# Optimization experiments

Measured on AMD Instinct MI355X. Metric: run time of the kernel, lower is better.

The kernel has to match this reference:

```python
import jax, jax.numpy as jnp
import numpy as np
from jax import lax

WSIZE = 11
SIGMA = 1.5
PAD = WSIZE // 2  # 5
C1 = 0.01 ** 2
C2 = 0.03 ** 2


def _gauss1d():
    x = np.arange(WSIZE) - WSIZE // 2
    g = np.exp(-(x.astype(np.float64) ** 2) / (2.0 * SIGMA ** 2))
    g = g / g.sum()
    return jnp.asarray(g, dtype=jnp.float32)


def _blur3d(x, g):
    """Replicate-pad by 5 on D/H/W then apply the separable 11x11x11 Gaussian.
    x: [N, 1, D, H, W]. Mathematically identical to the dense conv3d in the
    original (the 3D window is an exact outer product of the 1D Gaussian)."""
    xp = jnp.pad(x, ((0, 0), (0, 0), (PAD, PAD), (PAD, PAD), (PAD, PAD)), mode='edge')
    dn = ('NCDHW', 'OIDHW', 'NCDHW')
    for kshape in ((1, 1, WSIZE, 1, 1), (1, 1, 1, WSIZE, 1), (1, 1, 1, 1, WSIZE)):
        xp = lax.conv_general_dilated(xp, g.reshape(kshape), (1, 1, 1), 'VALID',
                                      dimension_numbers=dn)
    return xp


def _rerange(img):
    img = jnp.where(img.max() > 128.0, img / 255.0, img)
    img = jnp.where(img.min() < -0.5, (img + 1.0) / 2.0, img)
    return img


def setup_inputs() -> dict:
    key = jax.random.key(0)
    k1, k2 = jax.random.split(key)
    N, C, H, W = 4, 16, 512, 512
    pred = jax.random.uniform(k1, (N, C, H, W), dtype=jnp.float32)
    gt = jax.random.uniform(k2, (N, C, H, W), dtype=jnp.float32)
    return {"pred": pred, "gt": gt}


def reference(pred, gt):
    N = pred.shape[0]
    pred = _rerange(pred)
    gt = _rerange(gt)

    # ---- PSNR (range = 1.0, reduce='sum') ----
    mse = jnp.mean((pred - gt) ** 2, axis=(1, 2, 3))           # [N]
    psnr = jnp.sum(10.0 * jnp.log10(1.0 / mse))                # scalar

    # ---- 3D SSIM over [N,1,C,H,W] volumes ----
    g = _gauss1d()
    img = pred[:, None]                                        # [N,1,D,H,W]
    gtt = gt[:, None]
    mu1 = _blur3d(img, g)
    mu2 = _blur3d(gtt, g)
    mu1_sq = mu1 * mu1
    mu2_sq = mu2 * mu2
    mu1_mu2 = mu1 * mu2
    sigma1_sq = _blur3d(img * img, g) - mu1_sq
    sigma2_sq = _blur3d(gtt * gtt, g) - mu2_sq
    sigma12 = _blur3d(img * gtt, g) - mu1_mu2

    v1 = 2.0 * sigma12 + C2
    v2 = sigma1_sq + sigma2_sq + C2
    ssim_map = ((2.0 * mu1_mu2 + C1) * v1) / ((mu1_sq + mu2_sq + C1) * v2)
    ssim = jnp.sum(jnp.mean(ssim_map, axis=(1, 2, 3, 4)))      # reduce='sum'

    return psnr, ssim, N
```

## Files before the change

### kernel.cpp

```cpp
#include <hip/hip_runtime.h>
#include <cmath>


#define NB 4
#define DD 16
#define HH 512
#define WW 512
#define SLICE (HH * WW)
#define VOL (DD * SLICE)
#define C1F 0.0001f
#define C2F 0.0009f

#define TH 16
#define TW 16
#define SCOLS 26
#define NRP 13
#define PW 14
#define PLSTR 28
#define SDW (NRP * PLSTR)
#define TMW (TH * PW)
#define NTHR 256
#define SIT (NRP * SCOLS)
#define XTRA (SIT - NTHR)
#define HITEMS 104

typedef _Float16 h2v __attribute__((ext_vector_type(2)));

struct KArg {
  unsigned ge[6], go[6];
  unsigned wl2[DD * DD];
};

__device__ inline float dot2h(unsigned a, unsigned b, float c) {
#if __has_builtin(__builtin_amdgcn_fdot2)
  return __builtin_amdgcn_fdot2(__builtin_bit_cast(h2v, a),
                                __builtin_bit_cast(h2v, b), c, false);
#else
  h2v av = __builtin_bit_cast(h2v, a), bv = __builtin_bit_cast(h2v, b);
  return fmaf((float)av.y, (float)bv.y, fmaf((float)av.x, (float)bv.x, c));
#endif
}
__device__ inline unsigned pkh(float a, float b) {
  return __builtin_bit_cast(unsigned, __builtin_amdgcn_cvt_pkrtz(a, b));
}
__device__ inline unsigned pk2sq(unsigned a) {
  h2v v = __builtin_bit_cast(h2v, a);
  v = v * v;
  return __builtin_bit_cast(unsigned, v);
}
__device__ inline int iclamp(int v, int lo, int hi) {
  return v < lo ? lo : (v > hi ? hi : v);
}

__device__ inline float block_sum256(float v) {
#pragma unroll
  for (int o = 32; o > 0; o >>= 1) v += __shfl_down(v, o, 64);
  __shared__ float r[4];
  if ((threadIdx.x & 63) == 0) r[threadIdx.x >> 6] = v;
  __syncthreads();
  float out = 0.f;
  if (threadIdx.x == 0) {
#pragma unroll
    for (int i = 0; i < 4; ++i) out += r[i];
  }
  __syncthreads();
  return out;
}

__global__ void zero_acc_k(float* acc) {
  if (threadIdx.x < 8) acc[threadIdx.x] = 0.f;
}

__global__ __launch_bounds__(NTHR, 3) void fused_k(
    const float* __restrict__ pred, const float* __restrict__ gt,
    float* __restrict__ acc, KArg ka) {
  __shared__ uint2 sd[SDW];
  __shared__ uint4 tmp[TMW];

  int b0 = blockIdx.x;
  int b = (b0 & 7) * ((NB * 1024) >> 3) + (b0 >> 3);
  int tile = b & 1023;
  int n = b >> 10;
  int th0 = (tile >> 5) * TH;
  int tw0 = (tile & 31) * TW;
  int t = threadIdx.x;

  int rp0 = t / SCOLS, x0 = t - rp0 * SCOLS;
  int gx0 = iclamp(tw0 + x0 - 5, 0, WW - 1);
  int go0a = iclamp(th0 + 2 * rp0 - 5, 0, HH - 1) * WW + gx0;
  int go0b = iclamp(th0 + 2 * rp0 - 4, 0, HH - 1) * WW + gx0;
  int w0i = (2 * rp0 + (x0 & 1)) * PW + (x0 >> 1);
  bool ox0 = (x0 >= 5) && (x0 < 5 + TW);
  float o0a = (ox0 && rp0 >= 3 && rp0 <= 10) ? 1.f : 0.f;
  float o0b = (ox0 && rp0 >= 2 && rp0 <= 9) ? 1.f : 0.f;
  int i1 = t + XTRA;
  bool has2 = (i1 >= NTHR);
  int rp1 = i1 / SCOLS, x1 = i1 - rp1 * SCOLS;
  int gx1 = iclamp(tw0 + x1 - 5, 0, WW - 1);
  int go1a = iclamp(th0 + 2 * rp1 - 5, 0, HH - 1) * WW + gx1;
  int go1b = iclamp(th0 + 2 * rp1 - 4, 0, HH - 1) * WW + gx1;
  int w1i = (2 * rp1 + (x1 & 1)) * PW + (x1 >> 1);
  bool ox1 = (x1 >= 5) && (x1 < 5 + TW);
  float o1a = (ox1 && rp1 >= 3 && rp1 <= 10) ? 1.f : 0.f;
  float o1b = (ox1 && rp1 >= 2 && rp1 <= 9) ? 1.f : 0.f;

  bool hasH = (t < HITEMS);
  int hm = t & 7, hcp = t >> 3;
  int hrd = hm * PLSTR + hcp;
  int hwr = (2 * hm) * PW + hcp;

  int wx = t & 15;
  int wrd = (t >> 4) * PW + (wx >> 1);
  unsigned cw[6];
#pragma unroll
  for (int J = 0; J < 6; ++J) cw[J] = (wx & 1) ? ka.go[J] : ka.ge[J];

  const float* pb = pred + (size_t)n * VOL;
  const float* qb = gt + (size_t)n * VOL;

  float p0a = pb[go0a], p0b = pb[go0b], q0a = qb[go0a], q0b = qb[go0b];
  float p1a = 0.f, p1b = 0.f, q1a = 0.f, q1b = 0.f;
  if (has2) { p1a = pb[go1a]; p1b = pb[go1b]; q1a = qb[go1a]; q1b = qb[go1b]; }

  float psnr = 0.f;
  h2v A01[DD], A23[DD];
#pragma unroll
  for (int j = 0; j < DD; ++j) {
    A01[j] = (h2v){(_Float16)0, (_Float16)0};
    A23[j] = (h2v){(_Float16)0, (_Float16)0};
  }

#pragma unroll 1
  for (int d = 0; d < DD; ++d) {
    {
      float SA = p0a + q0a, DA = p0a - q0a;
      float SB = p0b + q0b, DB = p0b - q0b;
      psnr = fmaf(o0a, DA * DA, psnr);
      psnr = fmaf(o0b, DB * DB, psnr);
      sd[w0i] = make_uint2(pkh(SA, SB), pkh(DA, DB));
    }
    if (has2) {
      float SA = p1a + q1a, DA = p1a - q1a;
      float SB = p1b + q1b, DB = p1b - q1b;
      psnr = fmaf(o1a, DA * DA, psnr);
      psnr = fmaf(o1b, DB * DB, psnr);
      sd[w1i] = make_uint2(pkh(SA, SB), pkh(DA, DB));
    }
    __syncthreads();

    if (d < DD - 1) {
      const float* P = pb + (size_t)(d + 1) * SLICE;
      const float* Q = qb + (size_t)(d + 1) * SLICE;
      p0a = P[go0a]; p0b = P[go0b]; q0a = Q[go0a]; q0b = Q[go0b];
      if (has2) { p1a = P[go1a]; p1b = P[go1b]; q1a = Q[go1a]; q1b = Q[go1b]; }
    }

    if (hasH) {
      float e0[4] = {0, 0, 0, 0}, e1[4] = {0, 0, 0, 0};
      float r0[4] = {0, 0, 0, 0}, r1[4] = {0, 0, 0, 0};
#pragma unroll
      for (int J = 0; J < 6; ++J) {
        uint2 ve = sd[hrd + J * PLSTR];
        uint2 vo = sd[hrd + J * PLSTR + PW];
        unsigned ves = pk2sq(ve.x), ved = pk2sq(ve.y);
        unsigned vos = pk2sq(vo.x), vod = pk2sq(vo.y);
        unsigned cge = ka.ge[J], cgo = ka.go[J];
        e0[0] = dot2h(cge, ve.x, e0[0]); e0[1] = dot2h(cge, ve.y, e0[1]);
        e0[2] = dot2h(cge, ves, e0[2]);  e0[3] = dot2h(cge, ved, e0[3]);
        r0[0] = dot2h(cgo, ve.x, r0[0]); r0[1] = dot2h(cgo, ve.y, r0[1]);
        r0[2] = dot2h(cgo, ves, r0[2]);  r0[3] = dot2h(cgo, ved, r0[3]);
        e1[0] = dot2h(cge, vo.x, e1[0]); e1[1] = dot2h(cge, vo.y, e1[1]);
        e1[2] = dot2h(cge, vos, e1[2]);  e1[3] = dot2h(cge, vod, e1[3]);
        r1[0] = dot2h(cgo, vo.x, r1[0]); r1[1] = dot2h(cgo, vo.y, r1[1]);
        r1[2] = dot2h(cgo, vos, r1[2]);  r1[3] = dot2h(cgo, vod, r1[3]);
      }
      tmp[hwr] = make_uint4(pkh(e0[0], e1[0]), pkh(e0[1], e1[1]),
                            pkh(e0[2], e1[2]), pkh(e0[3], e1[3]));
      tmp[hwr + PW] = make_uint4(pkh(r0[0], r1[0]), pkh(r0[1], r1[1]),
                                 pkh(r0[2], r1[2]), pkh(r0[3], r1[3]));
    }
    __syncthreads();

    float w0 = 0.f, w1 = 0.f, w2 = 0.f, w3 = 0.f;
#pragma unroll
    for (int J = 0; J < 6; ++J) {
      uint4 v = tmp[wrd + J];
      w0 = dot2h(cw[J], v.x, w0); w1 = dot2h(cw[J], v.y, w1);
      w2 = dot2h(cw[J], v.z, w2); w3 = dot2h(cw[J], v.w, w3);
    }
    h2v p01 = __builtin_bit_cast(h2v, pkh(w0, w1));
    h2v p23 = __builtin_bit_cast(h2v, pkh(w2, w3));
    const unsigned* wl = ka.wl2 + d * DD;
#pragma unroll
    for (int o = 0; o < DD; ++o) {
      h2v w = __builtin_bit_cast(h2v, wl[o]);
      A01[o] = __builtin_elementwise_fma(w, p01, A01[o]);
      A23[o] = __builtin_elementwise_fma(w, p23, A23[o]);
    }
  }

  float ssum = 0.f;
#pragma unroll
  for (int j = 0; j < DD; ++j) {
    float Sb = (float)A01[j].x, Db = (float)A01[j].y;
    float B1 = (float)A23[j].x, B2 = (float)A23[j].y;
    float SS = Sb * Sb, DDm = Db * Db;
    float m12_2 = (SS - DDm) * 0.5f;
    float msq   = (SS + DDm) * 0.5f;
    float Epq   = (B1 - B2) * 0.25f;
    float Esum  = (B1 + B2) * 0.5f;
    float sig12_2 = 2.f * Epq - m12_2;
    float svar    = Esum - msq;
    float num = (m12_2 + C1F) * (sig12_2 + C2F);
    float den = (msq + C1F) * (svar + C2F);
    ssum += num / den;
  }
  float bs = block_sum256(ssum);
  if (t == 0) atomicAdd(&acc[4 + n], bs);
  float bp = block_sum256(psnr);
  if (t == 0) atomicAdd(&acc[n], bp);
}

__global__ void final_k(const float* __restrict__ acc, float* __restrict__ out) {
  if (threadIdx.x == 0 && blockIdx.x == 0) {
    double psnr = 0.0, ssim = 0.0;
    for (int n = 0; n < NB; ++n) {
      double mse = (double)acc[n] / (double)VOL;
      psnr += 10.0 * log10(1.0 / mse);
      ssim += (double)acc[4 + n] / (double)VOL;
    }
    out[0] = (float)psnr;
    out[1] = (float)ssim;
    out[2] = (float)NB;
  }
}

static unsigned short f2h(float f) {
  union { float f; unsigned u; } v; v.f = f;
  unsigned u = v.u;
  unsigned s = (u >> 16) & 0x8000u;
  int e = (int)((u >> 23) & 0xff) - 127 + 15;
  unsigned m = u & 0x7fffffu;
  if (e <= 0) return (unsigned short)s;
  if (e >= 31) return (unsigned short)(s | 0x7c00u);
  unsigned h = ((unsigned)e << 10) | (m >> 13);
  unsigned rem = m & 0x1fffu;
  if (rem > 0x1000u || (rem == 0x1000u && (h & 1u))) h++;
  return (unsigned short)(s | h);
}
static float h2f(unsigned short h) {
  unsigned se = (h >> 10) & 0x1f, m = h & 0x3ffu, s = ((unsigned)h & 0x8000u) << 16;
  union { unsigned u; float f; } v;
  if (se == 0) { v.u = s; return v.f; }
  v.u = s | ((se - 15 + 127) << 23) | (m << 13);
  return v.f;
}

extern "C" void kernel_launch(void* const* d_in, const int* in_sizes, int n_in,
                              void* d_out, int out_size, void* d_ws, size_t ws_size,
                              hipStream_t stream) {
  const float* pred = (const float*)d_in[0];
  const float* gt = (const float*)d_in[1];
  float* acc = (float*)d_ws;

  double tt[11], s = 0.0;
  for (int i = 0; i < 11; ++i) {
    double x = i - 5;
    tt[i] = exp(-(x * x) / 4.5);
    s += tt[i];
  }
  float g[11];
  for (int i = 0; i < 11; ++i) g[i] = (float)(tt[i] / s);

  unsigned short hg[11];
  for (int i = 0; i < 11; ++i) hg[i] = f2h(g[i]);
  for (int pass = 0; pass < 3; ++pass) {
    double sum = 0.0;
    for (int i = 0; i < 11; ++i) sum += (double)h2f(hg[i]);
    hg[5] = f2h((float)((double)h2f(hg[5]) + (1.0 - sum)));
  }

  KArg ka;
  for (int j = 0; j < 5; ++j)
    ka.ge[j] = (unsigned)hg[2 * j] | ((unsigned)hg[2 * j + 1] << 16);
  ka.ge[5] = (unsigned)hg[10];
  ka.go[0] = ((unsigned)hg[0]) << 16;
  for (int j = 1; j < 6; ++j)
    ka.go[j] = (unsigned)hg[2 * j - 1] | ((unsigned)hg[2 * j] << 16);

  float wl[DD][DD];
  for (int o = 0; o < DD; ++o)
    for (int d = 0; d < DD; ++d) {
      float w = 0.f;
      for (int k = 0; k < 11; ++k) {
        int j = o + k - 5;
        j = j < 0 ? 0 : (j > 15 ? 15 : j);
        if (j == d) w += g[k];
      }
      wl[d][o] = w;
    }
  for (int o = 0; o < DD; ++o) {
    unsigned short wv[DD];
    int dmx = 0;
    for (int d = 0; d < DD; ++d) {
      wv[d] = f2h(wl[d][o]);
      if (wl[d][o] > wl[dmx][o]) dmx = d;
    }
    for (int pass = 0; pass < 3; ++pass) {
      double sum = 0.0;
      for (int d = 0; d < DD; ++d) sum += (double)h2f(wv[d]);
      wv[dmx] = f2h((float)((double)h2f(wv[dmx]) + (1.0 - sum)));
    }
    for (int d = 0; d < DD; ++d)
      ka.wl2[d * DD + o] = (unsigned)wv[d] | ((unsigned)wv[d] << 16);
  }

  zero_acc_k<<<1, 64, 0, stream>>>(acc);
  fused_k<<<NB * 1024, NTHR, 0, stream>>>(pred, gt, acc, ka);
  final_k<<<1, 1, 0, stream>>>(acc, (float*)d_out);
}
```

Before: 238.8 us.

## Process two depth slices per loop iteration to halve barriers

The depth loop now handles two slices per iteration, with doubled shared-memory staging buffers. The horizontal pass spreads 208 threads across both slices instead of 104 on one, so more threads do useful work, and the number of __syncthreads per slice is halved. Loads for the next two slices are issued together. In exchange, shared memory and register use per block grow, which may reduce occupancy below the launch-bounds target of 3 blocks.

```diff
diff --git a/kernel.cpp b/kernel.cpp
--- a/kernel.cpp
+++ b/kernel.cpp
@@ -74,8 +74,8 @@
 __global__ __launch_bounds__(NTHR, 3) void fused_k(
     const float* __restrict__ pred, const float* __restrict__ gt,
     float* __restrict__ acc, KArg ka) {
-  __shared__ uint2 sd[SDW];
-  __shared__ uint4 tmp[TMW];
+  __shared__ uint2 sd[2 * SDW];
+  __shared__ uint4 tmp[2 * TMW];
 
   int b0 = blockIdx.x;
   int b = (b0 & 7) * ((NB * 1024) >> 3) + (b0 >> 3);
@@ -104,10 +104,11 @@
   float o1a = (ox1 && rp1 >= 3 && rp1 <= 10) ? 1.f : 0.f;
   float o1b = (ox1 && rp1 >= 2 && rp1 <= 9) ? 1.f : 0.f;
 
-  bool hasH = (t < HITEMS);
-  int hm = t & 7, hcp = t >> 3;
-  int hrd = hm * PLSTR + hcp;
-  int hwr = (2 * hm) * PW + hcp;
+  bool hasH = (t < 2 * HITEMS);
+  int hs = t & 1, hi = t >> 1;
+  int hm = hi & 7, hcp = hi >> 3;
+  int hrd = hs * SDW + hm * PLSTR + hcp;
+  int hwr = hs * TMW + (2 * hm) * PW + hcp;
 
   int wx = t & 15;
   int wrd = (t >> 4) * PW + (wx >> 1);
@@ -118,9 +119,16 @@
   const float* pb = pred + (size_t)n * VOL;
   const float* qb = gt + (size_t)n * VOL;
 
-  float p0a = pb[go0a], p0b = pb[go0b], q0a = qb[go0a], q0b = qb[go0b];
-  float p1a = 0.f, p1b = 0.f, q1a = 0.f, q1b = 0.f;
-  if (has2) { p1a = pb[go1a]; p1b = pb[go1b]; q1a = qb[go1a]; q1b = qb[go1b]; }
+  float pa0a = pb[go0a], pa0b = pb[go0b], qa0a = qb[go0a], qa0b = qb[go0b];
+  float pb0a = pb[SLICE + go0a], pb0b = pb[SLICE + go0b];
+  float qb0a = qb[SLICE + go0a], qb0b = qb[SLICE + go0b];
+  float pa1a = 0.f, pa1b = 0.f, qa1a = 0.f, qa1b = 0.f;
+  float pb1a = 0.f, pb1b = 0.f, qb1a = 0.f, qb1b = 0.f;
+  if (has2) {
+    pa1a = pb[go1a]; pa1b = pb[go1b]; qa1a = qb[go1a]; qa1b = qb[go1b];
+    pb1a = pb[SLICE + go1a]; pb1b = pb[SLICE + go1b];
+    qb1a = qb[SLICE + go1a]; qb1b = qb[SLICE + go1b];
+  }
 
   float psnr = 0.f;
   h2v A01[DD], A23[DD];
@@ -131,28 +139,44 @@
   }
 
 #pragma unroll 1
-  for (int d = 0; d < DD; ++d) {
+  for (int dd = 0; dd < DD; dd += 2) {
     {
-      float SA = p0a + q0a, DA = p0a - q0a;
-      float SB = p0b + q0b, DB = p0b - q0b;
+      float SA = pa0a + qa0a, DA = pa0a - qa0a;
+      float SB = pa0b + qa0b, DB = pa0b - qa0b;
       psnr = fmaf(o0a, DA * DA, psnr);
       psnr = fmaf(o0b, DB * DB, psnr);
       sd[w0i] = make_uint2(pkh(SA, SB), pkh(DA, DB));
+      SA = pb0a + qb0a; DA = pb0a - qb0a;
+      SB = pb0b + qb0b; DB = pb0b - qb0b;
+      psnr = fmaf(o0a, DA * DA, psnr);
+      psnr = fmaf(o0b, DB * DB, psnr);
+      sd[SDW + w0i] = make_uint2(pkh(SA, SB), pkh(DA, DB));
     }
     if (has2) {
-      float SA = p1a + q1a, DA = p1a - q1a;
-      float SB = p1b + q1b, DB = p1b - q1b;
+      float SA = pa1a + qa1a, DA = pa1a - qa1a;
+      float SB = pa1b + qa1b, DB = pa1b - qa1b;
       psnr = fmaf(o1a, DA * DA, psnr);
       psnr = fmaf(o1b, DB * DB, psnr);
       sd[w1i] = make_uint2(pkh(SA, SB), pkh(DA, DB));
+      SA = pb1a + qb1a; DA = pb1a - qb1a;
+      SB = pb1b + qb1b; DB = pb1b - qb1b;
+      psnr = fmaf(o1a, DA * DA, psnr);
+      psnr = fmaf(o1b, DB * DB, psnr);
+      sd[SDW + w1i] = make_uint2(pkh(SA, SB), pkh(DA, DB));
     }
     __syncthreads();
 
-    if (d < DD - 1) {
-      const float* P = pb + (size_t)(d + 1) * SLICE;
-      const float* Q = qb + (size_t)(d + 1) * SLICE;
-      p0a = P[go0a]; p0b = P[go0b]; q0a = Q[go0a]; q0b = Q[go0b];
-      if (has2) { p1a = P[go1a]; p1b = P[go1b]; q1a = Q[go1a]; q1b = Q[go1b]; }
+    if (dd < DD - 2) {
+      const float* PA = pb + (size_t)(dd + 2) * SLICE;
+      const float* QA = qb + (size_t)(dd + 2) * SLICE;
+      pa0a = PA[go0a]; pa0b = PA[go0b]; qa0a = QA[go0a]; qa0b = QA[go0b];
+      const float* PB = pb + (size_t)(dd + 3) * SLICE;
+      const float* QB = qb + (size_t)(dd + 3) * SLICE;
+      pb0a = PB[go0a]; pb0b = PB[go0b]; qb0a = QB[go0a]; qb0b = QB[go0b];
+      if (has2) {
+        pa1a = PA[go1a]; pa1b = PA[go1b]; qa1a = QA[go1a]; qa1b = QA[go1b];
+        pb1a = PB[go1a]; pb1b = PB[go1b]; qb1a = QB[go1a]; qb1b = QB[go1b];
+      }
     }
 
     if (hasH) {
@@ -181,21 +205,41 @@
     }
     __syncthreads();
 
-    float w0 = 0.f, w1 = 0.f, w2 = 0.f, w3 = 0.f;
-#pragma unroll
-    for (int J = 0; J < 6; ++J) {
-      uint4 v = tmp[wrd + J];
-      w0 = dot2h(cw[J], v.x, w0); w1 = dot2h(cw[J], v.y, w1);
-      w2 = dot2h(cw[J], v.z, w2); w3 = dot2h(cw[J], v.w, w3);
-    }
-    h2v p01 = __builtin_bit_cast(h2v, pkh(w0, w1));
-    h2v p23 = __builtin_bit_cast(h2v, pkh(w2, w3));
-    const unsigned* wl = ka.wl2 + d * DD;
-#pragma unroll
-    for (int o = 0; o < DD; ++o) {
-      h2v w = __builtin_bit_cast(h2v, wl[o]);
-      A01[o] = __builtin_elementwise_fma(w, p01, A01[o]);
-      A23[o] = __builtin_elementwise_fma(w, p23, A23[o]);
+    {
+      float w0 = 0.f, w1 = 0.f, w2 = 0.f, w3 = 0.f;
+#pragma unroll
+      for (int J = 0; J < 6; ++J) {
+        uint4 v = tmp[wrd + J];
+        w0 = dot2h(cw[J], v.x, w0); w1 = dot2h(cw[J], v.y, w1);
+        w2 = dot2h(cw[J], v.z, w2); w3 = dot2h(cw[J], v.w, w3);
+      }
+      h2v p01 = __builtin_bit_cast(h2v, pkh(w0, w1));
+      h2v p23 = __builtin_bit_cast(h2v, pkh(w2, w3));
+      const unsigned* wl = ka.wl2 + dd * DD;
+#pragma unroll
+      for (int o = 0; o < DD; ++o) {
+        h2v w = __builtin_bit_cast(h2v, wl[o]);
+        A01[o] = __builtin_elementwise_fma(w, p01, A01[o]);
+        A23[o] = __builtin_elementwise_fma(w, p23, A23[o]);
+      }
+    }
+    {
+      float w0 = 0.f, w1 = 0.f, w2 = 0.f, w3 = 0.f;
+#pragma unroll
+      for (int J = 0; J < 6; ++J) {
+        uint4 v = tmp[TMW + wrd + J];
+        w0 = dot2h(cw[J], v.x, w0); w1 = dot2h(cw[J], v.y, w1);
+        w2 = dot2h(cw[J], v.z, w2); w3 = dot2h(cw[J], v.w, w3);
+      }
+      h2v p01 = __builtin_bit_cast(h2v, pkh(w0, w1));
+      h2v p23 = __builtin_bit_cast(h2v, pkh(w2, w3));
+      const unsigned* wl = ka.wl2 + (dd + 1) * DD;
+#pragma unroll
+      for (int o = 0; o < DD; ++o) {
+        h2v w = __builtin_bit_cast(h2v, wl[o]);
+        A01[o] = __builtin_elementwise_fma(w, p01, A01[o]);
+        A23[o] = __builtin_elementwise_fma(w, p23, A23[o]);
+      }
     }
   }
 
```

Result: no change. 237.2 us (-0.6%).
